# Kernel tuning notes

Hardware: AMD Instinct MI355X
Metric: run time of the kernel (lower is better)

The kernel has to match this reference:

```python
import jax, jax.numpy as jnp
import numpy as np

N, C = 50000, 91
K_PRE = 1000            # pre-NMS top-k candidates (fixed shape for jit)
DET_PER_IMG = 100
SCORE_THRESH = 0.05
NMS_THRESH = 0.5
MIN_SIZE = 0.01
LOG_SCALE_CLAMP = float(np.log(1000.0 / 16.0))  # torchvision BoxCoder clamp
BBOX_W = (10.0, 10.0, 5.0, 5.0)


def setup_inputs() -> dict:
    key = jax.random.key(0)
    k1, k2, k3, k4, k5, k6 = jax.random.split(key, 6)
    class_logits = jax.random.normal(k1, (N, C), jnp.float32) * 2.0
    box_regression = jax.random.normal(k2, (N, C * 4), jnp.float32) * 0.5
    x1 = jax.random.uniform(k3, (N,), jnp.float32) * 1200.0
    y1 = jax.random.uniform(k4, (N,), jnp.float32) * 700.0
    w = jax.random.uniform(k5, (N,), jnp.float32) * 150.0 + 4.0
    h = jax.random.uniform(k6, (N,), jnp.float32) * 150.0 + 4.0
    proposals = jnp.stack([x1, y1, x1 + w, y1 + h], axis=1)
    return {"class_logits": class_logits, "box_regression": box_regression,
            "proposals": proposals, "image_h": 800, "image_w": 1333}


def _decode(rel, props):
    # torchvision BoxCoder.decode_single with weights (10,10,5,5)
    wx, wy, ww, wh = BBOX_W
    pw = props[:, 2] - props[:, 0]
    ph = props[:, 3] - props[:, 1]
    cx = props[:, 0] + 0.5 * pw
    cy = props[:, 1] + 0.5 * ph
    dx = rel[:, 0] / wx
    dy = rel[:, 1] / wy
    dw = jnp.minimum(rel[:, 2] / ww, LOG_SCALE_CLAMP)
    dh = jnp.minimum(rel[:, 3] / wh, LOG_SCALE_CLAMP)
    pcx = dx * pw + cx
    pcy = dy * ph + cy
    ppw = jnp.exp(dw) * pw
    pph = jnp.exp(dh) * ph
    return jnp.stack([pcx - 0.5 * ppw, pcy - 0.5 * pph,
                      pcx + 0.5 * ppw, pcy + 0.5 * pph], axis=1)


def _iou_matrix(b):
    # b: [K,4] -> [K,K] pairwise IoU
    area = jnp.maximum(b[:, 2] - b[:, 0], 0.0) * jnp.maximum(b[:, 3] - b[:, 1], 0.0)
    lt = jnp.maximum(b[:, None, :2], b[None, :, :2])
    rb = jnp.minimum(b[:, None, 2:], b[None, :, 2:])
    wh = jnp.maximum(rb - lt, 0.0)
    inter = wh[..., 0] * wh[..., 1]
    return inter / (area[:, None] + area[None, :] - inter + 1e-7)


def _postprocess(class_logits, box_regression, proposals, image_h, image_w):
    num_classes = class_logits.shape[-1]
    n = proposals.shape[0]
    props = jnp.broadcast_to(proposals[:, None, :], (n, num_classes, 4)).reshape(-1, 4)
    boxes = _decode(box_regression.reshape(-1, 4), props)       # [N*C, 4]
    # clip_boxes_to_image
    boxes = jnp.stack([
        jnp.clip(boxes[:, 0], 0.0, float(image_w)),
        jnp.clip(boxes[:, 1], 0.0, float(image_h)),
        jnp.clip(boxes[:, 2], 0.0, float(image_w)),
        jnp.clip(boxes[:, 3], 0.0, float(image_h)),
    ], axis=1)
    scores = jax.nn.softmax(class_logits, axis=-1)               # [N, C]
    # drop background class 0
    boxes = boxes.reshape(n, num_classes, 4)[:, 1:].reshape(-1, 4)    # [N*(C-1), 4]
    scores = scores[:, 1:].reshape(-1)                                # [N*(C-1)]
    labels = jnp.broadcast_to(jnp.arange(1, num_classes), (n, num_classes - 1)).reshape(-1)
    # score threshold + remove small boxes -> mask (fixed-shape)
    w = boxes[:, 2] - boxes[:, 0]
    h = boxes[:, 3] - boxes[:, 1]
    valid = (scores > SCORE_THRESH) & (w >= MIN_SIZE) & (h >= MIN_SIZE)
    masked_scores = jnp.where(valid, scores, -1.0)
    s_k, idx = jax.lax.top_k(masked_scores, K_PRE)               # pre-NMS candidates
    b_k = boxes[idx]
    l_k = labels[idx]
    keep0 = s_k > 0.0
    # batched NMS via per-class coordinate offset
    offset = l_k.astype(b_k.dtype) * float(image_w + image_h + 2)
    iou = _iou_matrix(b_k + offset[:, None])                     # [K,K]
    ar = jnp.arange(K_PRE)
    def body(i, keep):
        sup = keep[i] & (iou[i] > NMS_THRESH) & (ar > i)
        return keep & ~sup
    keep = jax.lax.fori_loop(0, K_PRE, body, keep0)
    final_scores = jnp.where(keep, s_k, -1.0)
    s_out, j = jax.lax.top_k(final_scores, DET_PER_IMG)
    ok = s_out > 0.0
    boxes_out = jnp.where(ok[:, None], b_k[j], 0.0)
    scores_out = jnp.where(ok, s_out, 0.0)
    labels_out = jnp.where(ok, l_k[j], 0)
    return boxes_out, scores_out, labels_out


def reference(class_logits, box_regression, proposals, image_h, image_w):
    return _postprocess(class_logits, box_regression, proposals, image_h, image_w)
```

## Files before the change

kernel.cpp:

```cpp
#include <hip/hip_runtime.h>
#include <cstdint>

#define NROWS 50000
#define NCLS  91
#define KPRE  1000
#define NDET  100
#define CAP   4096
#define BIN_OFF 62770u
#define LOGCLAMP 4.135166556742356f
#define P1BLK 3125
#define R2BLK 196
#define NFINE 256
#define NU4   6250
#define GCHUNK 128

constexpr size_t OFF_CNT     = 0;
constexpr size_t OFF_ROWMAX  = 64;
constexpr size_t OFF_COMPACT = 100096;
constexpr size_t OFF_SSCORE  = 132864;
constexpr size_t OFF_SGIDX   = 136960;
constexpr size_t OFF_SLABEL  = 141056;
constexpr size_t OFF_BRAW    = 145152;
constexpr size_t OFF_BNMS    = 161536;
constexpr size_t OFF_MASK    = 177920;

__device__ __forceinline__ bool decode_box(int row, int c,
    const float* __restrict__ regr, const float* __restrict__ props,
    float W, float H, float4& b) {
  const float4 rr = *reinterpret_cast<const float4*>(regr + (size_t)row * (NCLS * 4) + c * 4);
  const float4 pp = *reinterpret_cast<const float4*>(props + (size_t)row * 4);
  float pw = pp.z - pp.x, ph = pp.w - pp.y;
  float cx = pp.x + 0.5f * pw, cy = pp.y + 0.5f * ph;
  float dx = rr.x / 10.0f, dy = rr.y / 10.0f;
  float dw = fminf(rr.z / 5.0f, LOGCLAMP);
  float dh = fminf(rr.w / 5.0f, LOGCLAMP);
  float pcx = dx * pw + cx, pcy = dy * ph + cy;
  float ppw = expf(dw) * pw, pph = expf(dh) * ph;
  float x1 = fminf(fmaxf(pcx - 0.5f * ppw, 0.f), W);
  float y1 = fminf(fmaxf(pcy - 0.5f * pph, 0.f), H);
  float x2 = fminf(fmaxf(pcx + 0.5f * ppw, 0.f), W);
  float y2 = fminf(fmaxf(pcy + 0.5f * pph, 0.f), H);
  b = make_float4(x1, y1, x2, y2);
  return (x2 - x1 >= 0.01f) && (y2 - y1 >= 0.01f);
}

__global__ __launch_bounds__(256)
void pass1_kernel(const float* __restrict__ logits,
                  const float* __restrict__ regr,
                  const float* __restrict__ props,
                  const int* __restrict__ p_imh,
                  const int* __restrict__ p_imw,
                  uint16_t* __restrict__ rowmax,
                  uint32_t* __restrict__ cnt) {
  if (blockIdx.x == 0 && threadIdx.x == 0) cnt[1] = 0;
  const int gt  = blockIdx.x * 256 + threadIdx.x;
  const int row = gt >> 4;
  const int sub = gt & 15;
  const float* lr = logits + (size_t)row * NCLS;

  float x[6];
  #pragma unroll
  for (int j = 0; j < 6; ++j) {
    int c = sub + 16 * j;
    x[j] = (c < NCLS) ? lr[c] : -INFINITY;
  }
  float m = x[0];
  #pragma unroll
  for (int j = 1; j < 6; ++j) m = fmaxf(m, x[j]);
  m = fmaxf(m, __shfl_xor(m, 1));
  m = fmaxf(m, __shfl_xor(m, 2));
  m = fmaxf(m, __shfl_xor(m, 4));
  m = fmaxf(m, __shfl_xor(m, 8));
  float e[6]; float s = 0.f;
  #pragma unroll
  for (int j = 0; j < 6; ++j) {
    e[j] = (sub + 16 * j < NCLS) ? expf(x[j] - m) : 0.f;
    s += e[j];
  }
  s += __shfl_xor(s, 1);
  s += __shfl_xor(s, 2);
  s += __shfl_xor(s, 4);
  s += __shfl_xor(s, 8);

  const float W = (float)(*p_imw), H = (float)(*p_imh);
  int maxbin = 0;
  #pragma unroll
  for (int j = 0; j < 6; ++j) {
    int c = sub + 16 * j;
    if (c >= 1 && c < NCLS) {
      float score = e[j] / s;
      if (score > 0.05f) {
        float4 b;
        if (decode_box(row, c, regr, props, W, H, b)) {
          uint32_t bin = (__float_as_uint(score) >> 14) - BIN_OFF;
          if ((int)bin > maxbin) maxbin = (int)bin;
        }
      }
    }
  }
  maxbin = max(maxbin, __shfl_xor(maxbin, 1));
  maxbin = max(maxbin, __shfl_xor(maxbin, 2));
  maxbin = max(maxbin, __shfl_xor(maxbin, 4));
  maxbin = max(maxbin, __shfl_xor(maxbin, 8));
  if (sub == 0) rowmax[row] = (uint16_t)maxbin;
}

__global__ __launch_bounds__(256)
void refine_kernel(const float* __restrict__ logits,
                   const float* __restrict__ regr,
                   const float* __restrict__ props,
                   const int* __restrict__ p_imh,
                   const int* __restrict__ p_imw,
                   const uint16_t* __restrict__ rowmax,
                   uint32_t* __restrict__ cnt,
                   unsigned long long* __restrict__ compact) {
  __shared__ uint32_t fine[NFINE + 1];
  __shared__ uint32_t cw[4][9];
  __shared__ uint32_t ctot[9];
  __shared__ uint32_t s_cut;
  const int t = threadIdx.x;
  const int lane = t & 63;
  const int wv = t >> 6;

  const uint4* r128 = reinterpret_cast<const uint4*>(rowmax);
  unsigned long long acc = 0ull;
  uint32_t c8 = 0;
  for (int k = t; k < NU4; k += 256) {
    uint4 v = r128[k];
    #pragma unroll
    for (int w = 0; w < 4; ++w) {
      uint32_t u = (w == 0) ? v.x : (w == 1) ? v.y : (w == 2) ? v.z : v.w;
      uint32_t a = u & 0xffffu, b = u >> 16;
      if (a) { uint32_t ba = a >> 8; if (ba < 8u) acc += 1ull << (8u * ba); else ++c8; }
      if (b) { uint32_t bb = b >> 8; if (bb < 8u) acc += 1ull << (8u * bb); else ++c8; }
    }
  }
  uint32_t cc[9];
  #pragma unroll
  for (int q = 0; q < 8; ++q) cc[q] = (uint32_t)((acc >> (8 * q)) & 0xffull);
  cc[8] = c8;
  #pragma unroll
  for (int off = 32; off; off >>= 1) {
    #pragma unroll
    for (int q = 0; q < 9; ++q) cc[q] += __shfl_xor(cc[q], off);
  }
  if (lane == 0) {
    #pragma unroll
    for (int q = 0; q < 9; ++q) cw[wv][q] = cc[q];
  }
  if (t == 0) s_cut = 0xFFFFFFFFu;
  __syncthreads();
  if (t < 9) ctot[t] = cw[0][t] + cw[1][t] + cw[2][t] + cw[3][t];
  __syncthreads();
  uint32_t sfx[10];
  sfx[9] = 0;
  #pragma unroll
  for (int q = 8; q >= 0; --q) sfx[q] = sfx[q + 1] + ctot[q];
  const uint32_t total = sfx[0];
  if (total != 0) {
    const uint32_t target = total < (uint32_t)KPRE ? total : (uint32_t)KPRE;
    int Bc = 0;
    uint32_t S_hi = 0;
    #pragma unroll
    for (int q = 8; q >= 0; --q) {
      if (sfx[q] >= target && sfx[q + 1] < target) { Bc = q; S_hi = sfx[q + 1]; }
    }
    if (t < NFINE + 1) fine[t] = 0;
    __syncthreads();
    const uint32_t lo = (uint32_t)Bc << 8;
    for (int k = t; k < NU4; k += 256) {
      uint4 v = r128[k];
      #pragma unroll
      for (int w = 0; w < 4; ++w) {
        uint32_t u = (w == 0) ? v.x : (w == 1) ? v.y : (w == 2) ? v.z : v.w;
        uint32_t a = u & 0xffffu, b = u >> 16;
        if (a && (a >> 8) == (uint32_t)Bc) atomicAdd(&fine[a & 255u], 1u);
        if (b && (b >> 8) == (uint32_t)Bc) atomicAdd(&fine[b & 255u], 1u);
      }
    }
    __syncthreads();
    for (int off = 1; off < NFINE; off <<= 1) {
      uint32_t add = (t + off < NFINE) ? fine[t + off] : 0;
      __syncthreads();
      fine[t] += add;
      __syncthreads();
    }
    uint32_t hi = S_hi + fine[t];
    uint32_t hin = S_hi + ((t < NFINE - 1) ? fine[t + 1] : 0);
    if (hi >= target && hin < target) s_cut = lo + (uint32_t)t;
    __syncthreads();
  }
  const uint32_t cut = s_cut;

  const int g16 = lane >> 4;
  const int sub = lane & 15;
  const float W = (float)(*p_imw), H = (float)(*p_imh);
  const int base = blockIdx.x * 256;
  const int myrow0 = base + t;
  bool qual = (myrow0 < NROWS) && ((uint32_t)rowmax[myrow0] >= cut);
  unsigned long long bm = __ballot(qual);
  if (!bm) return;
  const int waveBase = base + (t & ~63);
  while (bm) {
    int bsel[4];
    #pragma unroll
    for (int k = 0; k < 4; ++k) {
      bsel[k] = bm ? (__ffsll((unsigned long long)bm) - 1) : -1;
      if (bm) bm &= bm - 1;
    }
    const int myb = bsel[g16];
    const int row = waveBase + (myb >= 0 ? myb : 0);
    const float* lr = logits + (size_t)row * NCLS;
    float x[6];
    #pragma unroll
    for (int j = 0; j < 6; ++j) {
      int c = sub + 16 * j;
      x[j] = (c < NCLS) ? lr[c] : -INFINITY;
    }
    float m = x[0];
    #pragma unroll
    for (int j = 1; j < 6; ++j) m = fmaxf(m, x[j]);
    m = fmaxf(m, __shfl_xor(m, 1));
    m = fmaxf(m, __shfl_xor(m, 2));
    m = fmaxf(m, __shfl_xor(m, 4));
    m = fmaxf(m, __shfl_xor(m, 8));
    float e[6]; float s = 0.f;
    #pragma unroll
    for (int j = 0; j < 6; ++j) {
      e[j] = (sub + 16 * j < NCLS) ? expf(x[j] - m) : 0.f;
      s += e[j];
    }
    s += __shfl_xor(s, 1);
    s += __shfl_xor(s, 2);
    s += __shfl_xor(s, 4);
    s += __shfl_xor(s, 8);
    if (myb >= 0) {
      #pragma unroll
      for (int j = 0; j < 6; ++j) {
        int c = sub + 16 * j;
        if (c >= 1 && c < NCLS) {
          float score = e[j] / s;
          if (score > 0.05f) {
            float4 bb;
            if (decode_box(row, c, regr, props, W, H, bb)) {
              uint32_t bits = __float_as_uint(score);
              uint32_t bin = (bits >> 14) - BIN_OFF;
              if (bin >= cut) {
                uint32_t pos = atomicAdd(&cnt[1], 1u);
                if (pos < CAP) {
                  uint32_t gidx = (uint32_t)row * 90u + (uint32_t)(c - 1);
                  compact[pos] = ((unsigned long long)bits << 32) |
                                 (unsigned long long)(0xFFFFFFFFu - gidx);
                }
              }
            }
          }
        }
      }
    }
  }
}

__global__ __launch_bounds__(1024)
void sort_prep_kernel(const unsigned long long* __restrict__ compact,
                      const uint32_t* __restrict__ cnt,
                      const float* __restrict__ regr, const float* __restrict__ props,
                      const int* __restrict__ p_imh, const int* __restrict__ p_imw,
                      float* __restrict__ sel_score, uint32_t* __restrict__ sel_gidx,
                      int* __restrict__ slabel, float4* __restrict__ braw,
                      float4* __restrict__ bnms) {
  __shared__ unsigned long long arr[CAP];
  const int t = threadIdx.x;
  const uint32_t M = cnt[1] < (uint32_t)CAP ? cnt[1] : (uint32_t)CAP;
  int P = 1024;
  while (P < (int)M) P <<= 1;
  for (int i = t; i < P; i += 1024) arr[i] = (i < (int)M) ? compact[i] : 0ull;
  __syncthreads();
  for (int k = 2; k <= P; k <<= 1) {
    for (int j = k >> 1; j > 0; j >>= 1) {
      for (int i = t; i < P; i += 1024) {
        int l = i ^ j;
        if (l > i) {
          unsigned long long A = arr[i], B = arr[l];
          bool up = ((i & k) == 0);
          if (up ? (A > B) : (A < B)) { arr[i] = B; arr[l] = A; }
        }
      }
      __syncthreads();
    }
  }
  if (t < KPRE) {
    unsigned long long en = arr[P - 1 - t];
    float sc; uint32_t g;
    if (en) { sc = __uint_as_float((uint32_t)(en >> 32)); g = 0xFFFFFFFFu - (uint32_t)en; }
    else    { sc = -1.f; g = 0xFFFFFFFFu; }
    sel_score[t] = sc;
    sel_gidx[t] = g;
    if (sc > 0.f) {
      int row = (int)(g / 90u);
      int c   = (int)(g % 90u) + 1;
      float W = (float)(*p_imw), H = (float)(*p_imh);
      float4 b;
      decode_box(row, c, regr, props, W, H, b);
      braw[t] = b;
      float offv = (float)c * (float)(*p_imw + *p_imh + 2);
      bnms[t] = make_float4(b.x + offv, b.y + offv, b.z + offv, b.w + offv);
      slabel[t] = c;
    } else {
      braw[t] = make_float4(0, 0, 0, 0);
      bnms[t] = make_float4(0, 0, 0, 0);
      slabel[t] = 0;
    }
  }
}

__global__ __launch_bounds__(256)
void iou_kernel(const float4* __restrict__ bnms, unsigned long long* __restrict__ mask) {
  const int i = blockIdx.x;
  const int lane = threadIdx.x & 63;
  const int wv = threadIdx.x >> 6;
  const float4 bi = bnms[i];
  const float areai = fmaxf(bi.z - bi.x, 0.f) * fmaxf(bi.w - bi.y, 0.f);
  #pragma unroll
  for (int ww = 0; ww < 4; ++ww) {
    int wd = wv * 4 + ww;
    int j = wd * 64 + lane;
    bool bit = false;
    if (j < KPRE && j > i) {
      float4 bj = bnms[j];
      float areaj = fmaxf(bj.z - bj.x, 0.f) * fmaxf(bj.w - bj.y, 0.f);
      float ltx = fmaxf(bi.x, bj.x), lty = fmaxf(bi.y, bj.y);
      float rbx = fminf(bi.z, bj.z), rby = fminf(bi.w, bj.w);
      float iw = fmaxf(rbx - ltx, 0.f), ih = fmaxf(rby - lty, 0.f);
      float inter = iw * ih;
      float iou = inter / (areai + areaj - inter + 1e-7f);
      bit = iou > 0.5f;
    }
    unsigned long long mword = __ballot(bit);
    if (lane == 0) mask[(size_t)i * 16 + wd] = mword;
  }
}

__global__ __launch_bounds__(256)
void greedy_kernel(const unsigned long long* __restrict__ mask,
                   const float* __restrict__ sel_score,
                   const int* __restrict__ slabel,
                   const float4* __restrict__ braw,
                   float* __restrict__ out) {
  __shared__ ulonglong2 buf[2][GCHUNK * 8];
  __shared__ int kept[NDET];
  __shared__ int s_done;
  const int t = threadIdx.x;
  const int lane = t & 63;
  const int wv = t >> 6;
  const ulonglong2* gm2 = reinterpret_cast<const ulonglong2*>(mask);
  constexpr int NCHUNK = (KPRE + GCHUNK - 1) / GCHUNK;

  unsigned long long kw = 0ull;
  #pragma unroll
  for (int w = 0; w < 16; ++w) {
    int j = w * 64 + lane;
    bool b = (j < KPRE) && (sel_score[j] > 0.f);
    unsigned long long mword = __ballot(b);
    if (lane == w) kw = mword;
  }
  if (t == 0) s_done = 0;

  {
    int rows = (KPRE < GCHUNK) ? KPRE : GCHUNK;
    int n2 = rows * 8;
    for (int k = t; k < n2; k += 256) buf[0][k] = gm2[k];
  }
  __syncthreads();

  int kc = 0;
  for (int c = 0; c < NCHUNK; ++c) {
    if (wv > 0 && c + 1 < NCHUNK) {
      int rows = KPRE - (c + 1) * GCHUNK;
      if (rows > GCHUNK) rows = GCHUNK;
      int n2 = rows * 8;
      size_t gbase = (size_t)(c + 1) * GCHUNK * 8;
      for (int k = t - 64; k < n2; k += 192) buf[(c + 1) & 1][k] = gm2[gbase + k];
    }
    if (wv == 0) {
      const unsigned long long* bb =
          reinterpret_cast<const unsigned long long*>(buf[c & 1]);
      int rows = KPRE - c * GCHUNK;
      if (rows > GCHUNK) rows = GCHUNK;
      unsigned long long curm = (lane < 16) ? bb[lane] : 0ull;
      for (int r = 0; r < rows; ++r) {
        unsigned long long nxt =
            (lane < 16 && r + 1 < rows) ? bb[(r + 1) * 16 + lane] : 0ull;
        int i = c * GCHUNK + r;
        unsigned long long kwv = __shfl(kw, i >> 6);
        if ((kwv >> (i & 63)) & 1ull) {
          if (lane == 0) kept[kc] = i;
          kw &= ~curm;
          ++kc;
          if (kc >= NDET) { if (lane == 0) s_done = 1; break; }
        }
        curm = nxt;
      }
    }
    __syncthreads();
    if (s_done) break;
  }

  if (wv == 0) {
    for (int q = lane; q < NDET; q += 64) {
      if (q < kc) {
        int i = kept[q];
        float4 b = braw[i];
        out[q * 4 + 0] = b.x; out[q * 4 + 1] = b.y;
        out[q * 4 + 2] = b.z; out[q * 4 + 3] = b.w;
        out[4 * NDET + q] = sel_score[i];
        out[5 * NDET + q] = (float)slabel[i];
      } else {
        out[q * 4 + 0] = 0.f; out[q * 4 + 1] = 0.f;
        out[q * 4 + 2] = 0.f; out[q * 4 + 3] = 0.f;
        out[4 * NDET + q] = 0.f;
        out[5 * NDET + q] = 0.f;
      }
    }
  }
}

extern "C" void kernel_launch(void* const* d_in, const int* in_sizes, int n_in,
                              void* d_out, int out_size, void* d_ws, size_t ws_size,
                              hipStream_t stream) {
  const float* logits = (const float*)d_in[0];
  const float* regr   = (const float*)d_in[1];
  const float* props  = (const float*)d_in[2];
  const int*   p_imh  = (const int*)d_in[3];
  const int*   p_imw  = (const int*)d_in[4];
  float* out = (float*)d_out;

  uint8_t* ws = (uint8_t*)d_ws;
  uint32_t* cnt  = (uint32_t*)(ws + OFF_CNT);
  uint16_t* rowmax = (uint16_t*)(ws + OFF_ROWMAX);
  unsigned long long* compact = (unsigned long long*)(ws + OFF_COMPACT);
  float*    sel_score = (float*)(ws + OFF_SSCORE);
  uint32_t* sel_gidx  = (uint32_t*)(ws + OFF_SGIDX);
  int*      slabel    = (int*)(ws + OFF_SLABEL);
  float4*   braw      = (float4*)(ws + OFF_BRAW);
  float4*   bnms      = (float4*)(ws + OFF_BNMS);
  unsigned long long* mask = (unsigned long long*)(ws + OFF_MASK);

  pass1_kernel<<<P1BLK, 256, 0, stream>>>(
      logits, regr, props, p_imh, p_imw, rowmax, cnt);
  refine_kernel<<<R2BLK, 256, 0, stream>>>(
      logits, regr, props, p_imh, p_imw, rowmax, cnt, compact);
  sort_prep_kernel<<<1, 1024, 0, stream>>>(compact, cnt, regr, props, p_imh, p_imw,
                                           sel_score, sel_gidx, slabel, braw, bnms);
  iou_kernel<<<KPRE, 256, 0, stream>>>(bnms, mask);
  greedy_kernel<<<1, 256, 0, stream>>>(mask, sel_score, slabel, braw, out);
}
```

Baseline: 107.2 us.

## Build coarse histogram in pass1 and enlarge refine blocks to 1024 threads

Pass1 now builds a per-block 9-bucket coarse histogram of row-max bins in LDS and writes it to a partial-count buffer. Refine reduces these partials instead of rescanning the whole rowmax array per block for the coarse histogram. Refine blocks also grow from 256 to 1024 threads with a quarter as many blocks, which cuts the redundant per-block fine-histogram scan. This trades extra LDS atomics and a small write in pass1, plus lower block-level parallelism in refine, for less duplicated global reading.

```diff
diff --git a/kernel.cpp b/kernel.cpp
--- a/kernel.cpp
+++ b/kernel.cpp
@@ -9,9 +9,11 @@
 #define BIN_OFF 62770u
 #define LOGCLAMP 4.135166556742356f
 #define P1BLK 3125
-#define R2BLK 196
+#define R2BLK 49
 #define NFINE 256
 #define NU4   6250
+#define CPS   3136
+#define CP4   3528
 #define GCHUNK 128
 
 constexpr size_t OFF_CNT     = 0;
@@ -23,6 +25,7 @@
 constexpr size_t OFF_BRAW    = 145152;
 constexpr size_t OFF_BNMS    = 161536;
 constexpr size_t OFF_MASK    = 177920;
+constexpr size_t OFF_CPART   = 305920;
 
 __device__ __forceinline__ bool decode_box(int row, int c,
     const float* __restrict__ regr, const float* __restrict__ props,
@@ -51,9 +54,15 @@
                   const int* __restrict__ p_imh,
                   const int* __restrict__ p_imw,
                   uint16_t* __restrict__ rowmax,
+                  uint16_t* __restrict__ cpart,
                   uint32_t* __restrict__ cnt) {
-  if (blockIdx.x == 0 && threadIdx.x == 0) cnt[1] = 0;
-  const int gt  = blockIdx.x * 256 + threadIdx.x;
+  __shared__ uint32_t lds9[9];
+  const int t = threadIdx.x;
+  if (blockIdx.x == 0 && t == 0) cnt[1] = 0;
+  if (t < 9) lds9[t] = 0;
+  __syncthreads();
+
+  const int gt  = blockIdx.x * 256 + t;
   const int row = gt >> 4;
   const int sub = gt & 15;
   const float* lr = logits + (size_t)row * NCLS;
@@ -102,62 +111,52 @@
   maxbin = max(maxbin, __shfl_xor(maxbin, 2));
   maxbin = max(maxbin, __shfl_xor(maxbin, 4));
   maxbin = max(maxbin, __shfl_xor(maxbin, 8));
-  if (sub == 0) rowmax[row] = (uint16_t)maxbin;
-}
-
-__global__ __launch_bounds__(256)
+  if (sub == 0) {
+    rowmax[row] = (uint16_t)maxbin;
+    if (maxbin > 0) atomicAdd(&lds9[maxbin >> 8], 1u);
+  }
+  __syncthreads();
+  if (t < 9) cpart[(size_t)t * CPS + blockIdx.x] = (uint16_t)lds9[t];
+  if (blockIdx.x < 9 && t < CPS - P1BLK)
+    cpart[(size_t)blockIdx.x * CPS + P1BLK + t] = 0;
+}
+
+__global__ __launch_bounds__(1024)
 void refine_kernel(const float* __restrict__ logits,
                    const float* __restrict__ regr,
                    const float* __restrict__ props,
                    const int* __restrict__ p_imh,
                    const int* __restrict__ p_imw,
                    const uint16_t* __restrict__ rowmax,
+                   const uint16_t* __restrict__ cpart,
                    uint32_t* __restrict__ cnt,
                    unsigned long long* __restrict__ compact) {
   __shared__ uint32_t fine[NFINE + 1];
-  __shared__ uint32_t cw[4][9];
-  __shared__ uint32_t ctot[9];
+  __shared__ uint32_t lds9[9];
   __shared__ uint32_t s_cut;
   const int t = threadIdx.x;
-  const int lane = t & 63;
-  const int wv = t >> 6;
-
-  const uint4* r128 = reinterpret_cast<const uint4*>(rowmax);
-  unsigned long long acc = 0ull;
-  uint32_t c8 = 0;
-  for (int k = t; k < NU4; k += 256) {
-    uint4 v = r128[k];
-    #pragma unroll
-    for (int w = 0; w < 4; ++w) {
-      uint32_t u = (w == 0) ? v.x : (w == 1) ? v.y : (w == 2) ? v.z : v.w;
-      uint32_t a = u & 0xffffu, b = u >> 16;
-      if (a) { uint32_t ba = a >> 8; if (ba < 8u) acc += 1ull << (8u * ba); else ++c8; }
-      if (b) { uint32_t bb = b >> 8; if (bb < 8u) acc += 1ull << (8u * bb); else ++c8; }
-    }
-  }
-  uint32_t cc[9];
-  #pragma unroll
-  for (int q = 0; q < 8; ++q) cc[q] = (uint32_t)((acc >> (8 * q)) & 0xffull);
-  cc[8] = c8;
-  #pragma unroll
-  for (int off = 32; off; off >>= 1) {
-    #pragma unroll
-    for (int q = 0; q < 9; ++q) cc[q] += __shfl_xor(cc[q], off);
-  }
-  if (lane == 0) {
-    #pragma unroll
-    for (int q = 0; q < 9; ++q) cw[wv][q] = cc[q];
-  }
+  if (t < 9) lds9[t] = 0;
+  if (t < NFINE + 1) fine[t] = 0;
   if (t == 0) s_cut = 0xFFFFFFFFu;
   __syncthreads();
-  if (t < 9) ctot[t] = cw[0][t] + cw[1][t] + cw[2][t] + cw[3][t];
+
+  const uint4* cp4 = reinterpret_cast<const uint4*>(cpart);
+  for (int k = t; k < CP4; k += 1024) {
+    uint4 v = cp4[k];
+    uint32_t ssum = (v.x & 0xffffu) + (v.x >> 16) + (v.y & 0xffffu) + (v.y >> 16) +
+                    (v.z & 0xffffu) + (v.z >> 16) + (v.w & 0xffffu) + (v.w >> 16);
+    if (ssum) atomicAdd(&lds9[k / 392], ssum);
+  }
   __syncthreads();
   uint32_t sfx[10];
   sfx[9] = 0;
   #pragma unroll
-  for (int q = 8; q >= 0; --q) sfx[q] = sfx[q + 1] + ctot[q];
+  for (int q = 8; q >= 0; --q) sfx[q] = sfx[q + 1] + lds9[q];
   const uint32_t total = sfx[0];
-  if (total != 0) {
+  uint32_t cut;
+  if (total == 0) {
+    cut = 0xFFFFFFFFu;
+  } else {
     const uint32_t target = total < (uint32_t)KPRE ? total : (uint32_t)KPRE;
     int Bc = 0;
     uint32_t S_hi = 0;
@@ -165,10 +164,8 @@
     for (int q = 8; q >= 0; --q) {
       if (sfx[q] >= target && sfx[q + 1] < target) { Bc = q; S_hi = sfx[q + 1]; }
     }
-    if (t < NFINE + 1) fine[t] = 0;
-    __syncthreads();
-    const uint32_t lo = (uint32_t)Bc << 8;
-    for (int k = t; k < NU4; k += 256) {
+    const uint4* r128 = reinterpret_cast<const uint4*>(rowmax);
+    for (int k = t; k < NU4; k += 1024) {
       uint4 v = r128[k];
       #pragma unroll
       for (int w = 0; w < 4; ++w) {
@@ -180,22 +177,25 @@
     }
     __syncthreads();
     for (int off = 1; off < NFINE; off <<= 1) {
-      uint32_t add = (t + off < NFINE) ? fine[t + off] : 0;
+      uint32_t add = (t < NFINE && t + off < NFINE) ? fine[t + off] : 0;
       __syncthreads();
-      fine[t] += add;
+      if (t < NFINE) fine[t] += add;
       __syncthreads();
     }
-    uint32_t hi = S_hi + fine[t];
-    uint32_t hin = S_hi + ((t < NFINE - 1) ? fine[t + 1] : 0);
-    if (hi >= target && hin < target) s_cut = lo + (uint32_t)t;
+    if (t < NFINE) {
+      uint32_t hi = S_hi + fine[t];
+      uint32_t hin = S_hi + ((t < NFINE - 1) ? fine[t + 1] : 0);
+      if (hi >= target && hin < target) s_cut = ((uint32_t)Bc << 8) + (uint32_t)t;
+    }
     __syncthreads();
-  }
-  const uint32_t cut = s_cut;
-
+    cut = s_cut;
+  }
+
+  const int lane = t & 63;
   const int g16 = lane >> 4;
   const int sub = lane & 15;
   const float W = (float)(*p_imw), H = (float)(*p_imh);
-  const int base = blockIdx.x * 256;
+  const int base = blockIdx.x * 1024;
   const int myrow0 = base + t;
   bool qual = (myrow0 < NROWS) && ((uint32_t)rowmax[myrow0] >= cut);
   unsigned long long bm = __ballot(qual);
@@ -445,11 +445,12 @@
   float4*   braw      = (float4*)(ws + OFF_BRAW);
   float4*   bnms      = (float4*)(ws + OFF_BNMS);
   unsigned long long* mask = (unsigned long long*)(ws + OFF_MASK);
+  uint16_t* cpart     = (uint16_t*)(ws + OFF_CPART);
 
   pass1_kernel<<<P1BLK, 256, 0, stream>>>(
-      logits, regr, props, p_imh, p_imw, rowmax, cnt);
-  refine_kernel<<<R2BLK, 256, 0, stream>>>(
-      logits, regr, props, p_imh, p_imw, rowmax, cnt, compact);
+      logits, regr, props, p_imh, p_imw, rowmax, cpart, cnt);
+  refine_kernel<<<R2BLK, 1024, 0, stream>>>(
+      logits, regr, props, p_imh, p_imw, rowmax, cpart, cnt, compact);
   sort_prep_kernel<<<1, 1024, 0, stream>>>(compact, cnt, regr, props, p_imh, p_imw,
                                            sel_score, sel_gidx, slabel, braw, bnms);
   iou_kernel<<<KPRE, 256, 0, stream>>>(bnms, mask);
```

Result: faster. 91.49 us (-14.7%).
